# Kernel optimization log

Measured on AMD Instinct MI355X. Metric: run time of the kernel, lower is better.

The kernel has to match this reference:

```python
import jax, jax.numpy as jnp
import numpy as np

N = 50000          # nodes
E_RAND = 1_600_000 # random edges (avg degree 32)
IN = 8             # in_features
OUT = 8            # out_features
B = 16             # batch columns of x
T = 5              # edge types AFTER add_self_loops (type 1 = self loop, 2..5 = original)


def setup_inputs() -> dict:
    key = jax.random.key(0)
    k1, k2, k3, k4, k5, k6 = jax.random.split(key, 6)
    x = jax.random.normal(k1, (N * IN, B), jnp.float32)
    loops = jnp.arange(N, dtype=jnp.int32)
    # self loops prepended (type 1), random edges with types 2..T (original types shifted +1)
    src = jnp.concatenate([loops, jax.random.randint(k2, (E_RAND,), 0, N, jnp.int32)])
    dst = jnp.concatenate([loops, jax.random.randint(k3, (E_RAND,), 0, N, jnp.int32)])
    edge_types = jnp.concatenate([
        jnp.ones(N, jnp.int32),
        jax.random.randint(k4, (E_RAND,), 2, T + 1, jnp.int32),
    ])
    bound = 1.0 / np.sqrt(IN)
    # weight_vector reshaped: expand() maps ext_type = ((e-1)*OUT + i)*IN + j + 1
    W = jax.random.uniform(k5, (T, OUT, IN), jnp.float32, -bound, bound)
    # bias_vector reshaped: expand(OUT, 1) -> per (type, out-row) scalar
    Bv = jax.random.uniform(k6, (T, OUT), jnp.float32, -bound, bound)
    return dict(x=x, W=W, Bv=Bv, src=src, dst=dst, edge_types=edge_types)


def reference(x, W, Bv, src, dst, edge_types):
    T_, OUT_, IN_ = W.shape
    Nn = x.shape[0] // IN_
    xr = x.reshape(Nn, IN_, -1)                 # [N, in, B]
    Wg = W[edge_types - 1]                      # [E, out, in] per-edge weight block gather
    msg = jnp.einsum('eoi,eib->eob', Wg, xr[src])  # [E, out, B]
    y = jax.ops.segment_sum(msg, dst, num_segments=Nn)            # [N, out, B]
    yb = jax.ops.segment_sum(Bv[edge_types - 1], dst, num_segments=Nn)  # [N, out]
    y = y + yb[:, :, None]
    return y.reshape(Nn * OUT_, -1)             # [N*out, B]
```

## Files before the change

kernel.cpp:

```cpp
#include <hip/hip_runtime.h>
#include <hip/hip_fp16.h>

#define N_NODES 50000
#define E_RAND  1600000
#define IN_F    8
#define OUT_F   8
#define BATCH   16

#define NB      391
#define CAP     4608
#define OSTRIDE 513
#define CHUNK   16384
#define NCHUNKS ((E_RAND + CHUNK - 1) / CHUNK)

#define OFF_BCUR   0
#define OFF_OFF    2048
#define OFF_XH     804864
#define OFF_BINNED 13604864
#define OFF_SORTED 20811776
#define WS_NEEDED  28018688

__global__ __launch_bounds__(256)
void convert_kernel(const float* __restrict__ x, __half* __restrict__ xh,
                    int* __restrict__ bcur) {
    if (blockIdx.x == 0)
        for (int i = threadIdx.x; i < NB; i += 256) bcur[i] = 0;
    const int b = threadIdx.x & 15;
    const int n = blockIdx.x * 16 + (threadIdx.x >> 4);
    if (n >= N_NODES) return;
    const float* xp = x + n * (IN_F * BATCH) + b;
    union { __half h[8]; uint4 u; } pk;
#pragma unroll
    for (int i = 0; i < IN_F; ++i) pk.h[i] = __float2half(xp[i * BATCH]);
    *(uint4*)(xh + (size_t)n * (IN_F * BATCH) + b * IN_F) = pk.u;
}

__global__ __launch_bounds__(512)
void binning_kernel(const int* __restrict__ src, const int* __restrict__ dst,
                    const int* __restrict__ et,
                    int* __restrict__ bcur, int* __restrict__ binned) {
    __shared__ int h[NB];
    __shared__ int base[NB];
    for (int i = threadIdx.x; i < NB; i += 512) h[i] = 0;
    __syncthreads();
    const int cbase = blockIdx.x * CHUNK;
#pragma unroll 4
    for (int k = 0; k < 32; ++k) {
        const int e = cbase + k * 512 + threadIdx.x;
        if (e < E_RAND) atomicAdd(&h[dst[N_NODES + e] >> 7], 1);
    }
    __syncthreads();
    for (int i = threadIdx.x; i < NB; i += 512) {
        const int c = h[i];
        base[i] = c ? atomicAdd(&bcur[i], c) : 0;
        h[i] = 0;
    }
    __syncthreads();
#pragma unroll 4
    for (int k = 0; k < 32; ++k) {
        const int e = cbase + k * 512 + threadIdx.x;
        if (e < E_RAND) {
            const int ee  = N_NODES + e;
            const int d   = dst[ee];
            const int bkt = d >> 7;
            const int payload = ((((d & 127) << 2) | (et[ee] - 2)) << 16) | src[ee];
            binned[bkt * CAP + base[bkt] + atomicAdd(&h[bkt], 1)] = payload;
        }
    }
}

__global__ __launch_bounds__(512)
void bucket_sort(const int* __restrict__ bcur, const int* __restrict__ binned,
                 int* __restrict__ off, int* __restrict__ sorted) {
    __shared__ int h[512];
    __shared__ int cur[512];
    const int bkt  = blockIdx.x;
    const int cnt  = bcur[bkt];
    const int base = bkt * CAP;
    const int t = threadIdx.x;
    h[t] = 0;
    __syncthreads();
    for (int i = t; i < cnt; i += 512)
        atomicAdd(&h[binned[base + i] >> 16], 1);
    __syncthreads();
    const int v = h[t];
    for (int d = 1; d < 512; d <<= 1) {
        __syncthreads();
        const int u = (t >= d) ? h[t - d] : 0;
        __syncthreads();
        h[t] += u;
    }
    __syncthreads();
    const int start = base + h[t] - v;
    off[bkt * OSTRIDE + t] = start;
    if (t == 511) off[bkt * OSTRIDE + 512] = base + cnt;
    cur[t] = start;
    __syncthreads();
    for (int i = t; i < cnt; i += 512) {
        const int p = binned[base + i];
        sorted[atomicAdd(&cur[p >> 16], 1)] = p & 0xFFFF;
    }
}

__device__ __forceinline__ void unpack_add(uint4 v, float* xa) {
    const __half2* hp = (const __half2*)&v;
    float2 f;
    f = __half22float2(hp[0]); xa[0] += f.x; xa[1] += f.y;
    f = __half22float2(hp[1]); xa[2] += f.x; xa[3] += f.y;
    f = __half22float2(hp[2]); xa[4] += f.x; xa[5] += f.y;
    f = __half22float2(hp[3]); xa[6] += f.x; xa[7] += f.y;
}

__global__ __launch_bounds__(256)
void gather_kernel(const __half* __restrict__ xh,
                   const float* __restrict__ W,
                   const float* __restrict__ Bv,
                   const int* __restrict__ off,
                   const int* __restrict__ sidx,
                   float* __restrict__ y) {
    const int lane = threadIdx.x & 63;
    const int n = blockIdx.x * 4 + (threadIdx.x >> 6);
    const int g = lane >> 4;
    const int b = lane & 15;
    const int o0 = g * 2;

    float out[2];
    {
        float xs[IN_F];
#pragma unroll
        for (int i = 0; i < IN_F; ++i) xs[i] = 0.f;
        unpack_add(*(const uint4*)(xh + (size_t)n * 128 + b * 8), xs);
#pragma unroll
        for (int c = 0; c < 2; ++c) {
            const int o = o0 + c;
            const float4 w0 = ((const float4*)(W + o * IN_F))[0];
            const float4 w1 = ((const float4*)(W + o * IN_F))[1];
            float a = Bv[o];
            a = fmaf(w0.x, xs[0], a); a = fmaf(w0.y, xs[1], a);
            a = fmaf(w0.z, xs[2], a); a = fmaf(w0.w, xs[3], a);
            a = fmaf(w1.x, xs[4], a); a = fmaf(w1.y, xs[5], a);
            a = fmaf(w1.z, xs[6], a); a = fmaf(w1.w, xs[7], a);
            out[c] = a;
        }
    }

    const int* offp = off + 4 * n + (n >> 7);
    int so[5];
#pragma unroll
    for (int j = 0; j < 5; ++j) so[j] = offp[j];

#pragma unroll
    for (int t = 0; t < 4; ++t) {
        const int s0 = so[t];
        const int s1 = so[t + 1];
        const int cnt = s1 - s0;
        if (cnt == 0) continue;

        float xa[IN_F];
#pragma unroll
        for (int i = 0; i < IN_F; ++i) xa[i] = 0.f;

        for (int e = s0 + g; e < s1; e += 4) {
            const int src = sidx[e];
            unpack_add(*(const uint4*)(xh + (size_t)src * 128 + b * 8), xa);
        }

#pragma unroll
        for (int i = 0; i < IN_F; ++i) {
            xa[i] += __shfl_xor(xa[i], 16);
            xa[i] += __shfl_xor(xa[i], 32);
        }

        const float* Wt = W + (t + 1) * (OUT_F * IN_F);
        const float* Bt = Bv + (t + 1) * OUT_F;
        const float fc = (float)cnt;
#pragma unroll
        for (int c = 0; c < 2; ++c) {
            const int o = o0 + c;
            const float4 w0 = ((const float4*)(Wt + o * IN_F))[0];
            const float4 w1 = ((const float4*)(Wt + o * IN_F))[1];
            float a = fmaf(fc, Bt[o], out[c]);
            a = fmaf(w0.x, xa[0], a); a = fmaf(w0.y, xa[1], a);
            a = fmaf(w0.z, xa[2], a); a = fmaf(w0.w, xa[3], a);
            a = fmaf(w1.x, xa[4], a); a = fmaf(w1.y, xa[5], a);
            a = fmaf(w1.z, xa[6], a); a = fmaf(w1.w, xa[7], a);
            out[c] = a;
        }
    }

    float* yp = y + n * (OUT_F * BATCH) + b;
    yp[(o0    ) * BATCH] = out[0];
    yp[(o0 + 1) * BATCH] = out[1];
}

__global__ __launch_bounds__(256)
void selfinit_kernel(const float* __restrict__ x,
                     const float* __restrict__ W,
                     const float* __restrict__ Bv,
                     float* __restrict__ y) {
    const int b = threadIdx.x & (BATCH - 1);
    const int n = blockIdx.x * 16 + (threadIdx.x >> 4);
    if (n >= N_NODES) return;
    float xc[IN_F];
#pragma unroll
    for (int i = 0; i < IN_F; ++i) xc[i] = x[(n * IN_F + i) * BATCH + b];
#pragma unroll
    for (int o = 0; o < OUT_F; ++o) {
        float a = Bv[o];
#pragma unroll
        for (int i = 0; i < IN_F; ++i) a = fmaf(W[o * IN_F + i], xc[i], a);
        y[(n * OUT_F + o) * BATCH + b] = a;
    }
}

__global__ __launch_bounds__(256)
void direct_edge_kernel(const float* __restrict__ x,
                        const float* __restrict__ W,
                        const float* __restrict__ Bv,
                        const int* __restrict__ src,
                        const int* __restrict__ dst,
                        const int* __restrict__ et,
                        float* __restrict__ y) {
    const int tid = blockIdx.x * 256 + threadIdx.x;
    const int eg  = tid >> 4;
    const int b   = tid & (BATCH - 1);
    if (eg >= E_RAND) return;
    const int e  = N_NODES + eg;
    const int s  = src[e];
    const int d  = dst[e];
    const int ti = et[e] - 1;
    const float* __restrict__ Wt = W + ti * (OUT_F * IN_F);
    float xc[IN_F];
#pragma unroll
    for (int i = 0; i < IN_F; ++i) xc[i] = x[(s * IN_F + i) * BATCH + b];
    float* yp = y + (size_t)d * (OUT_F * BATCH) + b;
#pragma unroll
    for (int o = 0; o < OUT_F; ++o) {
        float a = Bv[ti * OUT_F + o];
#pragma unroll
        for (int i = 0; i < IN_F; ++i) a = fmaf(Wt[o * IN_F + i], xc[i], a);
        unsafeAtomicAdd(yp + o * BATCH, a);
    }
}

extern "C" void kernel_launch(void* const* d_in, const int* in_sizes, int n_in,
                              void* d_out, int out_size, void* d_ws, size_t ws_size,
                              hipStream_t stream) {
    const float* x   = (const float*)d_in[0];
    const float* W   = (const float*)d_in[1];
    const float* Bv  = (const float*)d_in[2];
    const int*   src = (const int*)d_in[3];
    const int*   dst = (const int*)d_in[4];
    const int*   et  = (const int*)d_in[5];
    float* y = (float*)d_out;

    char* ws = (char*)d_ws;
    int*    bcur   = (int*)(ws + OFF_BCUR);
    int*    off    = (int*)(ws + OFF_OFF);
    __half* xh     = (__half*)(ws + OFF_XH);
    int*    binned = (int*)(ws + OFF_BINNED);
    int*    sorted = (int*)(ws + OFF_SORTED);

    if (ws_size >= WS_NEEDED) {
        convert_kernel<<<N_NODES / 16, 256, 0, stream>>>(x, xh, bcur);
        binning_kernel<<<NCHUNKS, 512, 0, stream>>>(src, dst, et, bcur, binned);
        bucket_sort<<<NB, 512, 0, stream>>>(bcur, binned, off, sorted);
        gather_kernel<<<N_NODES / 4, 256, 0, stream>>>(xh, W, Bv, off, sorted, y);
    } else {
        selfinit_kernel<<<(N_NODES + 15) / 16, 256, 0, stream>>>(x, W, Bv, y);
        direct_edge_kernel<<<(E_RAND * 16 + 255) / 256, 256, 0, stream>>>(x, W, Bv, src, dst, et, y);
    }
}
```

Measured before the change: 222.3 us.

## Fuse conversion and binning into one launch, shuffle-scan sort, prefetch gather

Merges the fp16 conversion and edge binning into a single heterogeneous launch (block ranges split by role) with smaller chunks for more binning blocks, and moves the bcur zeroing into a tiny separate kernel. The bucket sort's shared-memory Hillis-Steele scan is replaced by a wavefront shuffle scan plus per-wave totals, cutting barriers. The gather loop software-pipelines the index and row loads two edges ahead to hide latency. More global atomics on bcur from smaller chunks and an extra launch are the trade-offs.

```diff
diff --git a/kernel.cpp b/kernel.cpp
--- a/kernel.cpp
+++ b/kernel.cpp
@@ -10,8 +10,9 @@
 #define NB      391
 #define CAP     4608
 #define OSTRIDE 513
-#define CHUNK   16384
-#define NCHUNKS ((E_RAND + CHUNK - 1) / CHUNK)
+#define CHUNK   6144
+#define BIN_BLOCKS  ((E_RAND + CHUNK - 1) / CHUNK)
+#define CONV_BLOCKS 1563
 
 #define OFF_BCUR   0
 #define OFF_OFF    2048
@@ -20,51 +21,54 @@
 #define OFF_SORTED 20811776
 #define WS_NEEDED  28018688
 
-__global__ __launch_bounds__(256)
-void convert_kernel(const float* __restrict__ x, __half* __restrict__ xh,
-                    int* __restrict__ bcur) {
-    if (blockIdx.x == 0)
-        for (int i = threadIdx.x; i < NB; i += 256) bcur[i] = 0;
-    const int b = threadIdx.x & 15;
-    const int n = blockIdx.x * 16 + (threadIdx.x >> 4);
-    if (n >= N_NODES) return;
-    const float* xp = x + n * (IN_F * BATCH) + b;
-    union { __half h[8]; uint4 u; } pk;
-#pragma unroll
-    for (int i = 0; i < IN_F; ++i) pk.h[i] = __float2half(xp[i * BATCH]);
-    *(uint4*)(xh + (size_t)n * (IN_F * BATCH) + b * IN_F) = pk.u;
-}
-
 __global__ __launch_bounds__(512)
-void binning_kernel(const int* __restrict__ src, const int* __restrict__ dst,
-                    const int* __restrict__ et,
-                    int* __restrict__ bcur, int* __restrict__ binned) {
+void zero_kernel(int* __restrict__ p, int n) {
+    const int i = blockIdx.x * 512 + threadIdx.x;
+    if (i < n) p[i] = 0;
+}
+
+__global__ __launch_bounds__(512)
+void prep_kernel(const float* __restrict__ x, __half* __restrict__ xh,
+                 const int* __restrict__ src, const int* __restrict__ dst,
+                 const int* __restrict__ et,
+                 int* __restrict__ bcur, int* __restrict__ binned) {
+    if (blockIdx.x < CONV_BLOCKS) {
+        const int b = threadIdx.x & 15;
+        const int n = blockIdx.x * 32 + (threadIdx.x >> 4);
+        if (n >= N_NODES) return;
+        const float* xp = x + n * (IN_F * BATCH) + b;
+        union { __half h[8]; uint4 u; } pk;
+#pragma unroll
+        for (int i = 0; i < IN_F; ++i) pk.h[i] = __float2half(xp[i * BATCH]);
+        *(uint4*)(xh + (size_t)n * 128 + b * 8) = pk.u;
+        return;
+    }
     __shared__ int h[NB];
-    __shared__ int base[NB];
+    __shared__ int rbase[NB];
     for (int i = threadIdx.x; i < NB; i += 512) h[i] = 0;
     __syncthreads();
-    const int cbase = blockIdx.x * CHUNK;
+    const int cbase = (blockIdx.x - CONV_BLOCKS) * CHUNK;
 #pragma unroll 4
-    for (int k = 0; k < 32; ++k) {
+    for (int k = 0; k < CHUNK / 512; ++k) {
         const int e = cbase + k * 512 + threadIdx.x;
         if (e < E_RAND) atomicAdd(&h[dst[N_NODES + e] >> 7], 1);
     }
     __syncthreads();
     for (int i = threadIdx.x; i < NB; i += 512) {
         const int c = h[i];
-        base[i] = c ? atomicAdd(&bcur[i], c) : 0;
+        rbase[i] = c ? atomicAdd(&bcur[i], c) : 0;
         h[i] = 0;
     }
     __syncthreads();
 #pragma unroll 4
-    for (int k = 0; k < 32; ++k) {
+    for (int k = 0; k < CHUNK / 512; ++k) {
         const int e = cbase + k * 512 + threadIdx.x;
         if (e < E_RAND) {
             const int ee  = N_NODES + e;
             const int d   = dst[ee];
             const int bkt = d >> 7;
             const int payload = ((((d & 127) << 2) | (et[ee] - 2)) << 16) | src[ee];
-            binned[bkt * CAP + base[bkt] + atomicAdd(&h[bkt], 1)] = payload;
+            binned[bkt * CAP + rbase[bkt] + atomicAdd(&h[bkt], 1)] = payload;
         }
     }
 }
@@ -73,7 +77,7 @@
 void bucket_sort(const int* __restrict__ bcur, const int* __restrict__ binned,
                  int* __restrict__ off, int* __restrict__ sorted) {
     __shared__ int h[512];
-    __shared__ int cur[512];
+    __shared__ int wtot[8];
     const int bkt  = blockIdx.x;
     const int cnt  = bcur[bkt];
     const int base = bkt * CAP;
@@ -84,21 +88,25 @@
         atomicAdd(&h[binned[base + i] >> 16], 1);
     __syncthreads();
     const int v = h[t];
-    for (int d = 1; d < 512; d <<= 1) {
-        __syncthreads();
-        const int u = (t >= d) ? h[t - d] : 0;
-        __syncthreads();
-        h[t] += u;
-    }
-    __syncthreads();
-    const int start = base + h[t] - v;
+    const int lane = t & 63, wid = t >> 6;
+    int inc = v;
+#pragma unroll
+    for (int d = 1; d < 64; d <<= 1) {
+        const int u = __shfl_up(inc, d);
+        if (lane >= d) inc += u;
+    }
+    if (lane == 63) wtot[wid] = inc;
+    __syncthreads();
+    int wbase = 0;
+    for (int w = 0; w < wid; ++w) wbase += wtot[w];
+    const int start = base + wbase + inc - v;
+    h[t] = start;
     off[bkt * OSTRIDE + t] = start;
     if (t == 511) off[bkt * OSTRIDE + 512] = base + cnt;
-    cur[t] = start;
     __syncthreads();
     for (int i = t; i < cnt; i += 512) {
         const int p = binned[base + i];
-        sorted[atomicAdd(&cur[p >> 16], 1)] = p & 0xFFFF;
+        sorted[atomicAdd(&h[p >> 16], 1)] = p & 0xFFFF;
     }
 }
 
@@ -123,13 +131,14 @@
     const int g = lane >> 4;
     const int b = lane & 15;
     const int o0 = g * 2;
+    const int boff = b * 8;
 
     float out[2];
     {
         float xs[IN_F];
 #pragma unroll
         for (int i = 0; i < IN_F; ++i) xs[i] = 0.f;
-        unpack_add(*(const uint4*)(xh + (size_t)n * 128 + b * 8), xs);
+        unpack_add(*(const uint4*)(xh + (size_t)n * 128 + boff), xs);
 #pragma unroll
         for (int c = 0; c < 2; ++c) {
             const int o = o0 + c;
@@ -155,14 +164,21 @@
         const int s1 = so[t + 1];
         const int cnt = s1 - s0;
         if (cnt == 0) continue;
+        const int last = s1 - 1;
 
         float xa[IN_F];
 #pragma unroll
         for (int i = 0; i < IN_F; ++i) xa[i] = 0.f;
 
-        for (int e = s0 + g; e < s1; e += 4) {
-            const int src = sidx[e];
-            unpack_add(*(const uint4*)(xh + (size_t)src * 128 + b * 8), xa);
+        int e    = s0 + g;
+        int srcA = sidx[min(e, last)];
+        int srcB = sidx[min(e + 4, last)];
+        uint4 rowA = *(const uint4*)(xh + (size_t)srcA * 128 + boff);
+        while (e < s1) {
+            const uint4 rowB = *(const uint4*)(xh + (size_t)srcB * 128 + boff);
+            const int  srcC  = sidx[min(e + 8, last)];
+            unpack_add(rowA, xa);
+            rowA = rowB; srcB = srcC; e += 4;
         }
 
 #pragma unroll
@@ -262,8 +278,8 @@
     int*    sorted = (int*)(ws + OFF_SORTED);
 
     if (ws_size >= WS_NEEDED) {
-        convert_kernel<<<N_NODES / 16, 256, 0, stream>>>(x, xh, bcur);
-        binning_kernel<<<NCHUNKS, 512, 0, stream>>>(src, dst, et, bcur, binned);
+        zero_kernel<<<1, 512, 0, stream>>>(bcur, NB);
+        prep_kernel<<<CONV_BLOCKS + BIN_BLOCKS, 512, 0, stream>>>(x, xh, src, dst, et, bcur, binned);
         bucket_sort<<<NB, 512, 0, stream>>>(bcur, binned, off, sorted);
         gather_kernel<<<N_NODES / 4, 256, 0, stream>>>(xh, W, Bv, off, sorted, y);
     } else {
```

Measured after the change: 209.1 us. 6.0% less time.
